# Performance work log

Hardware: AMD Instinct MI355X
Metric: run time of the kernel (lower is better)

The kernel has to match this reference:

```python
import jax, jax.numpy as jnp
import numpy as np
import math

DIM = 768
FFN_DIM = 4 * DIM
EPS = 1e-5

def layer_norm(x, gamma, beta):
    mu = jnp.mean(x, axis=-1, keepdims=True)
    var = jnp.var(x, axis=-1, keepdims=True)
    return (x - mu) * jax.lax.rsqrt(var + EPS) * gamma + beta

def setup_inputs() -> dict:
    key = jax.random.key(0)
    ks = jax.random.split(key, 8)
    b, n, d = 8, 2048, DIM
    s = 1.0 / math.sqrt(d)
    x = jax.random.normal(ks[0], (b, n, d), dtype=jnp.float32)
    Wq = jax.random.normal(ks[1], (d, d), dtype=jnp.float32) * s
    Wk = jax.random.normal(ks[2], (d, d), dtype=jnp.float32) * s
    Wv = jax.random.normal(ks[3], (d, d), dtype=jnp.float32) * s
    W1 = jax.random.normal(ks[4], (d, FFN_DIM), dtype=jnp.float32) * s
    b1 = jnp.zeros((FFN_DIM,), dtype=jnp.float32)
    W2 = jax.random.normal(ks[5], (FFN_DIM, d), dtype=jnp.float32) * (1.0 / math.sqrt(FFN_DIM))
    b2 = jnp.zeros((d,), dtype=jnp.float32)
    g1 = jnp.ones((d,), dtype=jnp.float32); be1 = jnp.zeros((d,), dtype=jnp.float32)
    g2 = jnp.ones((d,), dtype=jnp.float32); be2 = jnp.zeros((d,), dtype=jnp.float32)
    return {"x": x, "Wq": Wq, "Wk": Wk, "Wv": Wv, "ln1_g": g1, "ln1_b": be1,
            "W1": W1, "b1": b1, "W2": W2, "b2": b2, "ln2_g": g2, "ln2_b": be2}

def reference(x, Wq, Wk, Wv, ln1_g, ln1_b, W1, b1, W2, b2, ln2_g, ln2_b):
    # Self-attention (single head, full dim; dropout in eval mode => identity)
    Q = jnp.einsum('bnd,de->bne', x, Wq)
    K = jnp.einsum('bnd,de->bne', x, Wk)
    V = jnp.einsum('bnd,de->bne', x, Wv)
    scores = jnp.einsum('bnd,bmd->bnm', Q, K) / math.sqrt(DIM)  # [b,n,n]
    attn = jax.nn.softmax(scores, axis=-1)
    O = jnp.einsum('bnm,bmd->bnd', attn, V)
    h = layer_norm(x + O, ln1_g, ln1_b)
    # FFN with exact GELU (torch nn.GELU default)
    hidden = jax.nn.gelu(jnp.einsum('bnd,df->bnf', h, W1) + b1, approximate=False)
    out = jnp.einsum('bnf,fd->bnd', hidden, W2) + b2
    return layer_norm(h + out, ln2_g, ln2_b)
```

## Files before the change

### kernel.cpp

```cpp
#include <hip/hip_runtime.h>
#include <hip/hip_bf16.h>
#include <math.h>

using u16 = unsigned short;
typedef __bf16 bf16x8 __attribute__((ext_vector_type(8)));
typedef float f32x4 __attribute__((ext_vector_type(4)));
typedef u16 u16x8 __attribute__((ext_vector_type(8)));

__device__ __forceinline__ u16 f2b(float f) {
  union { float f; unsigned u; } c; c.f = f;
  unsigned r = c.u + 0x7fffu + ((c.u >> 16) & 1u);
  return (u16)(r >> 16);
}
__device__ __forceinline__ float b2f(u16 h) {
  union { unsigned u; float f; } c; c.u = ((unsigned)h) << 16;
  return c.f;
}

__device__ __forceinline__ float fast_gelu(float t) {
  float y = fminf(1.5957691216f * t + 0.07135481283f * t * t * t, 80.f);
  float e = __expf(y);
  return t * e * (1.0f / (e + 1.0f));
}

#define EPI_BF16 0
#define EPI_EXP_SUM 1
#define EPI_GELU_BIAS 2
#define EPI_BF16_BIAS 4

#define GLDS16(src, dst)                                                     \
  __builtin_amdgcn_global_load_lds(                                          \
      (const __attribute__((address_space(1))) void*)(src),                  \
      (__attribute__((address_space(3))) void*)(dst), 16, 0, 0)

__device__ __forceinline__ int xswz(int o, int n) {
  int q = n >> 3, r = n & 7, x = o & 7, i = o >> 3;
  return (x < r ? x * (q + 1) : r * (q + 1) + (x - r) * q) + i;
}

template <int EPI>
__device__ __forceinline__ void epi_store(
    void* Cg, const float* bias, float v, long long off, int ccol, float scale)
{
  if (EPI == EPI_BF16) {
    ((u16*)Cg)[off] = f2b(v);
  } else if (EPI == EPI_GELU_BIAS) {
    ((u16*)Cg)[off] = f2b(fast_gelu(v + bias[ccol]));
  } else {
    ((u16*)Cg)[off] = f2b(v + bias[ccol]);
  }
}

template <int EPI>
__global__ __launch_bounds__(512, 4) void gemmW(
    const u16* __restrict__ Ag, const u16* __restrict__ Bg,
    void* __restrict__ Cg, const float* __restrict__ bias,
    int nbx, int K, float scale, int lda, int ldb, int ldc,
    long long sAz, long long sBz, long long sCz,
    float* __restrict__ lsum, int lzs)
{
  __shared__ __align__(16) u16 lds[24576];

  const int tid = threadIdx.x;
  const int wave = tid >> 6, lane = tid & 63;
  const int wr = wave >> 2, wc = wave & 3;
  const int id = xswz(blockIdx.x, gridDim.x);
  const int bx = id % nbx, by = id / nbx;
  const int m0 = by * 128, n0 = bx * 256;
  const long long z = blockIdx.z;
  const u16* A = Ag + z * sAz + (long long)m0 * lda;
  const u16* B = Bg + z * sBz + (long long)n0 * ldb;

  const int rA = wave * 16 + (lane >> 2);
  const int sA = (lane & 3) ^ ((rA >> 1) & 3);
  const u16* pa = A + (long long)rA * lda + sA * 8;
  const int rB = wave * 32 + (lane >> 2);
  const int sB = (lane & 3) ^ ((rB >> 1) & 3);
  const u16* pb0 = B + (long long)rB * ldb + sB * 8;
  const u16* pb1 = pb0 + (long long)16 * ldb;
  const int dA = wave * 512;
  const int dB0 = wave * 1024, dB1 = wave * 1024 + 512;

  int offA[4], offB[4];
#pragma unroll
  for (int f = 0; f < 4; ++f) {
    int ra = wr * 64 + f * 16 + (lane & 15);
    int ba = ra * 64 + ((lane >> 4) << 4);
    offA[f] = ba ^ (((ba >> 7) & 3) << 4);
    int rb = wc * 64 + f * 16 + (lane & 15);
    int bb = rb * 64 + ((lane >> 4) << 4);
    offB[f] = bb ^ (((bb >> 7) & 3) << 4);
  }

  f32x4 acc[4][4];
#pragma unroll
  for (int m = 0; m < 4; ++m)
#pragma unroll
    for (int n = 0; n < 4; ++n) acc[m][n] = f32x4{0.f, 0.f, 0.f, 0.f};

  const char* ldsc = (const char*)lds;
  const int NT = K >> 5;

  GLDS16(pa, lds + dA);
  GLDS16(pb0, lds + 4096 + dB0);
  GLDS16(pb1, lds + 4096 + dB1);
  asm volatile("s_waitcnt vmcnt(0)" ::: "memory");
  asm volatile("s_barrier" ::: "memory");

  for (int t = 0; t < NT; ++t) {
    const int kc = (t + 1 < NT ? t + 1 : 0) << 5;
    const char* cur = ldsc + (t & 1) * 24576;
    u16* nxt = lds + ((t & 1) ^ 1) * 12288;

    GLDS16(pa + kc, nxt + dA);
    GLDS16(pb0 + kc, nxt + 4096 + dB0);
    GLDS16(pb1 + kc, nxt + 4096 + dB1);

    bf16x8 Af[4], Bf[4];
#pragma unroll
    for (int f = 0; f < 4; ++f) {
      Af[f] = *(const bf16x8*)(cur + offA[f]);
      Bf[f] = *(const bf16x8*)(cur + 8192 + offB[f]);
    }
    __builtin_amdgcn_s_setprio(1);
#pragma unroll
    for (int m = 0; m < 4; ++m)
#pragma unroll
      for (int n = 0; n < 4; ++n)
        acc[m][n] = __builtin_amdgcn_mfma_f32_16x16x32_bf16(Af[m], Bf[n], acc[m][n], 0, 0, 0);
    __builtin_amdgcn_s_setprio(0);

    asm volatile("s_waitcnt vmcnt(0)" ::: "memory");
    asm volatile("s_barrier" ::: "memory");
  }

  if (EPI == EPI_EXP_SUM) {
#pragma unroll
    for (int mf = 0; mf < 4; ++mf) {
      const int crow = m0 + wr * 64 + mf * 16 + (lane >> 4) * 4;
      float part[4] = {0.f, 0.f, 0.f, 0.f};
#pragma unroll
      for (int nf = 0; nf < 4; ++nf) {
        const int ccol = n0 + wc * 64 + nf * 16 + (lane & 15);
#pragma unroll
        for (int j = 0; j < 4; ++j) {
          const float p = __expf(fminf(acc[mf][nf][j] * scale, 60.f));
          const u16 ub = f2b(p);
          ((u16*)Cg)[(long long)(crow + j) * ldc + ccol + z * sCz] = ub;
          part[j] += b2f(ub);
        }
      }
#pragma unroll
      for (int j = 0; j < 4; ++j) {
        float s = part[j];
        s += __shfl_xor(s, 1); s += __shfl_xor(s, 2);
        s += __shfl_xor(s, 4); s += __shfl_xor(s, 8);
        if ((lane & 15) == 0)
          atomicAdd(&lsum[(long long)z * lzs + crow + j], s);
      }
    }
  } else {
#pragma unroll
    for (int mf = 0; mf < 4; ++mf) {
#pragma unroll
      for (int nf = 0; nf < 4; ++nf) {
        const int crow = m0 + wr * 64 + mf * 16 + (lane >> 4) * 4;
        const int ccol = n0 + wc * 64 + nf * 16 + (lane & 15);
#pragma unroll
        for (int j = 0; j < 4; ++j) {
          const long long off = (long long)(crow + j) * ldc + ccol + z * sCz;
          epi_store<EPI>(Cg, bias, acc[mf][nf][j], off, ccol, scale);
        }
      }
    }
  }
}

__global__ __launch_bounds__(256) void zero_f32(float* __restrict__ p, int n) {
  const int i = blockIdx.x * 256 + threadIdx.x;
  if (i < n) p[i] = 0.f;
}

__global__ __launch_bounds__(256) void cast_f32_bf16(
    const float* __restrict__ x, u16* __restrict__ y, long long n4)
{
  const long long i = (long long)blockIdx.x * 256 + threadIdx.x;
  if (i >= n4) return;
  const float4 v = ((const float4*)x)[i];
  ushort4 o;
  o.x = f2b(v.x); o.y = f2b(v.y); o.z = f2b(v.z); o.w = f2b(v.w);
  ((ushort4*)y)[i] = o;
}

template <bool SRC_BF16>
__global__ __launch_bounds__(256) void transpose_cast(
    const void* __restrict__ srcv, u16* __restrict__ dst, int R, int C, int ldsrc,
    long long szSrc, long long szDst)
{
  __shared__ float tile[32][33];
  const long long zs = (long long)blockIdx.z * szSrc;
  const long long zd = (long long)blockIdx.z * szDst;
  const int c0 = blockIdx.x * 32, r0 = blockIdx.y * 32;
  const int tx = threadIdx.x & 31, ty = threadIdx.x >> 5;
#pragma unroll
  for (int i = 0; i < 4; ++i) {
    const int r = r0 + ty + i * 8;
    float v;
    if (SRC_BF16) v = b2f(((const u16*)srcv)[zs + (long long)r * ldsrc + c0 + tx]);
    else          v = ((const float*)srcv)[zs + (long long)r * ldsrc + c0 + tx];
    tile[ty + i * 8][tx] = v;
  }
  __syncthreads();
#pragma unroll
  for (int i = 0; i < 4; ++i) {
    const int c = c0 + ty + i * 8;
    dst[zd + (long long)c * R + r0 + tx] = f2b(tile[tx][ty + i * 8]);
  }
}

__global__ __launch_bounds__(256) void ln1_kernel(
    const u16* __restrict__ xb, const u16* __restrict__ O,
    const float* __restrict__ l,
    const float* __restrict__ g, const float* __restrict__ be,
    u16* __restrict__ h)
{
  __shared__ float red[8];
  const long long row = blockIdx.x;
  const u16* xr = xb + row * 768;
  const u16* orow = O + row * 768;
  const float invl = 1.0f / l[row];
  const int t = threadIdx.x, base = t * 3;

  float v[3];
#pragma unroll
  for (int j = 0; j < 3; ++j) v[j] = b2f(xr[base + j]) + b2f(orow[base + j]) * invl;
  float s = v[0] + v[1] + v[2];
  float ss = v[0] * v[0] + v[1] * v[1] + v[2] * v[2];
  for (int o = 32; o; o >>= 1) { s += __shfl_xor(s, o); ss += __shfl_xor(ss, o); }
  if ((t & 63) == 0) { red[t >> 6] = s; red[4 + (t >> 6)] = ss; }
  __syncthreads();
  s = red[0] + red[1] + red[2] + red[3];
  ss = red[4] + red[5] + red[6] + red[7];
  const float mu = s * (1.0f / 768.0f);
  const float var = ss * (1.0f / 768.0f) - mu * mu;
  const float inv = rsqrtf(var + 1e-5f);
#pragma unroll
  for (int j = 0; j < 3; ++j) {
    const float o = (v[j] - mu) * inv * g[base + j] + be[base + j];
    h[row * 768 + base + j] = f2b(o);
  }
}

__global__ __launch_bounds__(256) void ln2_kernel(
    const u16* __restrict__ h, const u16* __restrict__ ob,
    const float* __restrict__ g, const float* __restrict__ be,
    float* __restrict__ y)
{
  __shared__ float red[8];
  const long long row = blockIdx.x;
  const u16* hr = h + row * 768;
  const u16* orow = ob + row * 768;
  const int t = threadIdx.x, base = t * 3;

  float v[3];
#pragma unroll
  for (int j = 0; j < 3; ++j) v[j] = b2f(hr[base + j]) + b2f(orow[base + j]);
  float s = v[0] + v[1] + v[2];
  float ss = v[0] * v[0] + v[1] * v[1] + v[2] * v[2];
  for (int o = 32; o; o >>= 1) { s += __shfl_xor(s, o); ss += __shfl_xor(ss, o); }
  if ((t & 63) == 0) { red[t >> 6] = s; red[4 + (t >> 6)] = ss; }
  __syncthreads();
  s = red[0] + red[1] + red[2] + red[3];
  ss = red[4] + red[5] + red[6] + red[7];
  const float mu = s * (1.0f / 768.0f);
  const float var = ss * (1.0f / 768.0f) - mu * mu;
  const float inv = rsqrtf(var + 1e-5f);
#pragma unroll
  for (int j = 0; j < 3; ++j) {
    y[row * 768 + base + j] = (v[j] - mu) * inv * g[base + j] + be[base + j];
  }
}

extern "C" void kernel_launch(void* const* d_in, const int* in_sizes, int n_in,
                              void* d_out, int out_size, void* d_ws, size_t ws_size,
                              hipStream_t stream)
{
  const int Bb = 8, Nn = 2048, D = 768, F = 3072, E = 1536;
  const int M = Bb * Nn;
  const long long MD = (long long)M * D;

  const float* x   = (const float*)d_in[0];
  const float* Wq  = (const float*)d_in[1];
  const float* Wk  = (const float*)d_in[2];
  const float* Wv  = (const float*)d_in[3];
  const float* g1  = (const float*)d_in[4];
  const float* be1 = (const float*)d_in[5];
  const float* W1  = (const float*)d_in[6];
  const float* b1  = (const float*)d_in[7];
  const float* W2  = (const float*)d_in[8];
  const float* b2  = (const float*)d_in[9];
  const float* g2  = (const float*)d_in[10];
  const float* be2 = (const float*)d_in[11];

  u16* xb   = (u16*)d_out;
  u16* wqkt = xb + MD;
  u16* wvt  = wqkt + (size_t)E * D;

  char* w = (char*)d_ws;
  size_t off = 0;
  auto alloc = [&](size_t bytes) { void* p = w + off; off += bytes; return p; };
  u16* w1t = (u16*)alloc((size_t)F * D * 2);
  u16* w2t = (u16*)alloc((size_t)D * F * 2);
  u16* hb  = (u16*)alloc((size_t)MD * 2);
  float* lrow = (float*)alloc((size_t)M * 4);
  u16* qk  = (u16*)alloc((size_t)M * E * 2);
  u16* Vt  = (u16*)alloc((size_t)Bb * D * Nn * 2);
  u16* S   = (u16*)alloc((size_t)Bb * Nn * Nn * 2);
  u16* O   = (u16*)alloc((size_t)MD * 2);
  u16* hidden = qk;
  u16* outf   = qk + (size_t)M * F;

  const dim3 tcb(256);
  const float scl = 0.03608439182435161f;

  zero_f32<<<M / 256, 256, 0, stream>>>(lrow, M);
  cast_f32_bf16<<<(unsigned)(MD / 4 / 256), 256, 0, stream>>>(x, xb, MD / 4);
  transpose_cast<false><<<dim3(D / 32, D / 32, 1), tcb, 0, stream>>>(Wq, wqkt, D, D, D, 0, 0);
  transpose_cast<false><<<dim3(D / 32, D / 32, 1), tcb, 0, stream>>>(Wk, wqkt + D * D, D, D, D, 0, 0);
  transpose_cast<false><<<dim3(D / 32, D / 32, 1), tcb, 0, stream>>>(Wv, wvt, D, D, D, 0, 0);
  transpose_cast<false><<<dim3(F / 32, D / 32, 1), tcb, 0, stream>>>(W1, w1t, D, F, F, 0, 0);
  transpose_cast<false><<<dim3(D / 32, F / 32, 1), tcb, 0, stream>>>(W2, w2t, F, D, D, 0, 0);

  gemmW<EPI_BF16><<<dim3(6 * 128, 1, 1), 512, 0, stream>>>(
      xb, wqkt, qk, nullptr, 6, D, 1.f, D, D, E, 0, 0, 0, nullptr, 0);

  gemmW<EPI_BF16><<<dim3(8 * 6, 1, Bb), 512, 0, stream>>>(
      wvt, xb, Vt, nullptr, 8, D, 1.f, D, D, Nn,
      0, (long long)Nn * D, (long long)D * Nn, nullptr, 0);

  gemmW<EPI_EXP_SUM><<<dim3(8 * 16, 1, Bb), 512, 0, stream>>>(
      qk, qk + D, S, nullptr, 8, D, scl, E, E, Nn,
      (long long)Nn * E, (long long)Nn * E, (long long)Nn * Nn, lrow, Nn);

  gemmW<EPI_BF16><<<dim3(3 * 16, 1, Bb), 512, 0, stream>>>(
      S, Vt, O, nullptr, 3, Nn, 1.f, Nn, Nn, D,
      (long long)Nn * Nn, (long long)D * Nn, (long long)Nn * D, nullptr, 0);

  ln1_kernel<<<M, 256, 0, stream>>>(xb, O, lrow, g1, be1, hb);

  gemmW<EPI_GELU_BIAS><<<dim3(12 * 128, 1, 1), 512, 0, stream>>>(
      hb, w1t, hidden, b1, 12, D, 1.f, D, D, F, 0, 0, 0, nullptr, 0);

  gemmW<EPI_BF16_BIAS><<<dim3(3 * 128, 1, 1), 512, 0, stream>>>(
      hidden, w2t, outf, b2, 3, F, 1.f, F, F, D, 0, 0, 0, nullptr, 0);

  ln2_kernel<<<M, 256, 0, stream>>>(hb, outf, g2, be2, (float*)d_out);
}
```

Measured before the change: 470.3 us.

## Add 256x256-tile GEMM with 4-stage LDS pipeline for QK, scores, FFN1

Adds a new GEMM kernel that computes a 256x256 output tile per 512-thread block, using a 4-slot LDS ring (128 KB) with three K-tiles in flight, split A/B loads interleaved with two MFMA half-phases, and s_setprio around the MFMA bursts. It is used for the QK projection, the exp-score GEMM and the FFN1 GELU GEMM, halving block counts. The larger tiles raise operand reuse and cut global traffic per flop. The cost is lower occupancy (launch bounds 2, large LDS), more accumulator registers, and fewer blocks to spread across CUs.

```diff
diff --git a/kernel.cpp b/kernel.cpp
--- a/kernel.cpp
+++ b/kernel.cpp
@@ -48,6 +48,151 @@
     ((u16*)Cg)[off] = f2b(fast_gelu(v + bias[ccol]));
   } else {
     ((u16*)Cg)[off] = f2b(v + bias[ccol]);
+  }
+}
+
+template <int EPI>
+__global__ __launch_bounds__(512, 2) void gemm8p(
+    const u16* __restrict__ Ag, const u16* __restrict__ Bg,
+    void* __restrict__ Cg, const float* __restrict__ bias,
+    int nbx, int K, float scale, int lda, int ldb, int ldc,
+    long long sAz, long long sBz, long long sCz,
+    float* __restrict__ lsum, int lzs)
+{
+  __shared__ __align__(16) u16 lds[65536];
+
+  const int tid = threadIdx.x;
+  const int wave = tid >> 6, lane = tid & 63;
+  const int wr = wave >> 2, wc = wave & 3;
+  const int id = xswz(blockIdx.x, gridDim.x);
+  const int bx = id % nbx, by = id / nbx;
+  const int m0 = by * 256, n0 = bx * 256;
+  const long long z = blockIdx.z;
+  const u16* A = Ag + z * sAz + (long long)m0 * lda;
+  const u16* B = Bg + z * sBz + (long long)n0 * ldb;
+
+  const int rS = wave * 32 + (lane >> 2);
+  const int sS = (lane & 3) ^ ((rS >> 1) & 3);
+  const u16* pa0 = A + (long long)rS * lda + sS * 8;
+  const u16* pa1 = pa0 + (long long)16 * lda;
+  const u16* pb0 = B + (long long)rS * ldb + sS * 8;
+  const u16* pb1 = pb0 + (long long)16 * ldb;
+  const int dS0 = wave * 1024, dS1 = wave * 1024 + 512;
+
+  int offA[8], offB[4];
+#pragma unroll
+  for (int f = 0; f < 8; ++f) {
+    int ra = wr * 128 + f * 16 + (lane & 15);
+    int ba = ra * 64 + ((lane >> 4) << 4);
+    offA[f] = ba ^ (((ba >> 7) & 3) << 4);
+  }
+#pragma unroll
+  for (int f = 0; f < 4; ++f) {
+    int rb = wc * 64 + f * 16 + (lane & 15);
+    int bb = rb * 64 + ((lane >> 4) << 4);
+    offB[f] = bb ^ (((bb >> 7) & 3) << 4);
+  }
+
+  f32x4 acc[8][4];
+#pragma unroll
+  for (int m = 0; m < 8; ++m)
+#pragma unroll
+    for (int n = 0; n < 4; ++n) acc[m][n] = f32x4{0.f, 0.f, 0.f, 0.f};
+
+  const int NT = K >> 5;
+
+#pragma unroll
+  for (int s = 0; s < 3; ++s) {
+    u16* base = lds + s * 16384;
+    GLDS16(pa0 + s * 32, base + dS0);
+    GLDS16(pa1 + s * 32, base + dS1);
+    GLDS16(pb0 + s * 32, base + 8192 + dS0);
+    GLDS16(pb1 + s * 32, base + 8192 + dS1);
+  }
+  asm volatile("s_waitcnt vmcnt(8)" ::: "memory");
+  asm volatile("s_barrier" ::: "memory");
+
+  for (int t = 0; t < NT; ++t) {
+    const int tp3 = (t + 3 < NT) ? t + 3 : t + 3 - NT;
+    const int kc = tp3 << 5;
+    const char* cA = (const char*)(lds + (t & 3) * 16384);
+    const char* cB = cA + 16384;
+    u16* wslot = lds + ((t + 3) & 3) * 16384;
+
+    bf16x8 Af[4], Bf[4];
+
+    GLDS16(pa0 + kc, wslot + dS0);
+    GLDS16(pa1 + kc, wslot + dS1);
+#pragma unroll
+    for (int f = 0; f < 4; ++f) {
+      Af[f] = *(const bf16x8*)(cA + offA[f]);
+      Bf[f] = *(const bf16x8*)(cB + offB[f]);
+    }
+    asm volatile("s_barrier" ::: "memory");
+    __builtin_amdgcn_s_setprio(1);
+#pragma unroll
+    for (int m = 0; m < 4; ++m)
+#pragma unroll
+      for (int n = 0; n < 4; ++n)
+        acc[m][n] = __builtin_amdgcn_mfma_f32_16x16x32_bf16(Af[m], Bf[n], acc[m][n], 0, 0, 0);
+    __builtin_amdgcn_s_setprio(0);
+    asm volatile("s_barrier" ::: "memory");
+
+    GLDS16(pb0 + kc, wslot + 8192 + dS0);
+    GLDS16(pb1 + kc, wslot + 8192 + dS1);
+#pragma unroll
+    for (int f = 0; f < 4; ++f) Af[f] = *(const bf16x8*)(cA + offA[4 + f]);
+    asm volatile("s_barrier" ::: "memory");
+    __builtin_amdgcn_s_setprio(1);
+#pragma unroll
+    for (int m = 0; m < 4; ++m)
+#pragma unroll
+      for (int n = 0; n < 4; ++n)
+        acc[4 + m][n] = __builtin_amdgcn_mfma_f32_16x16x32_bf16(Af[m], Bf[n], acc[4 + m][n], 0, 0, 0);
+    __builtin_amdgcn_s_setprio(0);
+    asm volatile("s_waitcnt vmcnt(8)" ::: "memory");
+    asm volatile("s_barrier" ::: "memory");
+  }
+
+  if (EPI == EPI_EXP_SUM) {
+#pragma unroll
+    for (int mf = 0; mf < 8; ++mf) {
+      const int crow = m0 + wr * 128 + mf * 16 + (lane >> 4) * 4;
+      float part[4] = {0.f, 0.f, 0.f, 0.f};
+#pragma unroll
+      for (int nf = 0; nf < 4; ++nf) {
+        const int ccol = n0 + wc * 64 + nf * 16 + (lane & 15);
+#pragma unroll
+        for (int j = 0; j < 4; ++j) {
+          const float p = __expf(fminf(acc[mf][nf][j] * scale, 60.f));
+          const u16 ub = f2b(p);
+          ((u16*)Cg)[(long long)(crow + j) * ldc + ccol + z * sCz] = ub;
+          part[j] += b2f(ub);
+        }
+      }
+#pragma unroll
+      for (int j = 0; j < 4; ++j) {
+        float s = part[j];
+        s += __shfl_xor(s, 1); s += __shfl_xor(s, 2);
+        s += __shfl_xor(s, 4); s += __shfl_xor(s, 8);
+        if ((lane & 15) == 0)
+          atomicAdd(&lsum[(long long)z * lzs + crow + j], s);
+      }
+    }
+  } else {
+#pragma unroll
+    for (int mf = 0; mf < 8; ++mf) {
+#pragma unroll
+      for (int nf = 0; nf < 4; ++nf) {
+        const int crow = m0 + wr * 128 + mf * 16 + (lane >> 4) * 4;
+        const int ccol = n0 + wc * 64 + nf * 16 + (lane & 15);
+#pragma unroll
+        for (int j = 0; j < 4; ++j) {
+          const long long off = (long long)(crow + j) * ldc + ccol + z * sCz;
+          epi_store<EPI>(Cg, bias, acc[mf][nf][j], off, ccol, scale);
+        }
+      }
+    }
   }
 }
 
@@ -331,14 +476,14 @@
   transpose_cast<false><<<dim3(F / 32, D / 32, 1), tcb, 0, stream>>>(W1, w1t, D, F, F, 0, 0);
   transpose_cast<false><<<dim3(D / 32, F / 32, 1), tcb, 0, stream>>>(W2, w2t, F, D, D, 0, 0);
 
-  gemmW<EPI_BF16><<<dim3(6 * 128, 1, 1), 512, 0, stream>>>(
+  gemm8p<EPI_BF16><<<dim3(6 * 64, 1, 1), 512, 0, stream>>>(
       xb, wqkt, qk, nullptr, 6, D, 1.f, D, D, E, 0, 0, 0, nullptr, 0);
 
   gemmW<EPI_BF16><<<dim3(8 * 6, 1, Bb), 512, 0, stream>>>(
       wvt, xb, Vt, nullptr, 8, D, 1.f, D, D, Nn,
       0, (long long)Nn * D, (long long)D * Nn, nullptr, 0);
 
-  gemmW<EPI_EXP_SUM><<<dim3(8 * 16, 1, Bb), 512, 0, stream>>>(
+  gemm8p<EPI_EXP_SUM><<<dim3(8 * 8, 1, Bb), 512, 0, stream>>>(
       qk, qk + D, S, nullptr, 8, D, scl, E, E, Nn,
       (long long)Nn * E, (long long)Nn * E, (long long)Nn * Nn, lrow, Nn);
 
@@ -348,7 +493,7 @@
 
   ln1_kernel<<<M, 256, 0, stream>>>(xb, O, lrow, g1, be1, hb);
 
-  gemmW<EPI_GELU_BIAS><<<dim3(12 * 128, 1, 1), 512, 0, stream>>>(
+  gemm8p<EPI_GELU_BIAS><<<dim3(12 * 64, 1, 1), 512, 0, stream>>>(
       hb, w1t, hidden, b1, 12, D, 1.f, D, D, F, 0, 0, 0, nullptr, 0);
 
   gemmW<EPI_BF16_BIAS><<<dim3(3 * 128, 1, 1), 512, 0, stream>>>(
```

After: 480.3 us. +2.1%, slower.
